# Performance work log

Hardware: AMD Instinct MI355X
Metric: run time of the kernel (lower is better)

The kernel has to match this reference:

```python
import jax, jax.numpy as jnp
import numpy as np

N_VOLS, N_PARTS = 4, 8          # hard-coded in GL.forward
B = N_VOLS * N_PARTS            # asserted batch size = 32
DIM, HID, PROJ = 8192, 4096, 256
TEMP = 0.1
BN_EPS = 1e-5


def setup_inputs() -> dict:
    key = jax.random.key(0)
    k = jax.random.split(key, 5)
    s1 = 1.0 / np.sqrt(DIM)
    s2 = 1.0 / np.sqrt(HID)
    return {
        "x": jax.random.normal(k[0], (B, DIM), jnp.float32),
        "W1": jax.random.uniform(k[1], (DIM, HID), jnp.float32, -s1, s1),
        "b1": jax.random.uniform(k[2], (HID,), jnp.float32, -s1, s1),
        "gamma": jnp.ones((HID,), jnp.float32),
        "beta": jnp.zeros((HID,), jnp.float32),
        "W2": jax.random.uniform(k[3], (HID, PROJ), jnp.float32, -s2, s2),
        "b2": jax.random.uniform(k[4], (PROJ,), jnp.float32, -s2, s2),
    }


def _gl_loss(proj):
    # F.normalize(p=2, dim=-1); CosineSimilarity on unit vectors == dot product
    p = proj / jnp.linalg.norm(proj, axis=-1, keepdims=True)
    sims = (p @ p.T) / TEMP                       # [B, B]
    idx = jnp.arange(B)
    # pos_index(i) = {i % n_parts + v * n_parts} -> same part id; includes i itself
    pos_mask = (idx[:, None] % N_PARTS) == (idx[None, :] % N_PARTS)  # [B, B], 4 per row
    neg_mask = ~pos_mask                                             # 28 per row
    E = jnp.exp(sims)                              # original uses raw exp (no max-shift)
    row_neg = jnp.sum(jnp.where(neg_mask, E, 0.0), axis=1)    # sum_j exp(s[i, neg_j])
    ET = E.T                                        # ET[i, p] = exp(s[p, i])
    col_neg = jnp.sum(jnp.where(neg_mask, ET, 0.0), axis=1)   # sum_j exp(s[neg_j, i])
    t1 = -jnp.log(E / (E + row_neg[:, None]))      # row-direction term per (i, pos)
    t2 = -jnp.log(ET / (ET + col_neg[:, None]))    # column-direction term per (i, pos)
    per_row = jnp.sum(jnp.where(pos_mask, t1 + t2, 0.0), axis=1) / N_VOLS
    return jnp.sum(per_row) / (B * 2)


def reference(x, W1, b1, gamma, beta, W2, b2):
    # projector MLP: Linear -> BatchNorm1d (training stats) -> ReLU -> Linear
    h = x @ W1 + b1
    mu = jnp.mean(h, axis=0)
    var = jnp.var(h, axis=0)                       # biased variance, BN training mode
    h = gamma * (h - mu) * jax.lax.rsqrt(var + BN_EPS) + beta
    h = jax.nn.relu(h)
    proj = h @ W2 + b2                             # [B, PROJ]
    return _gl_loss(proj)
```

## Files before the change

### kernel.cpp

```cpp
#include <hip/hip_runtime.h>

#define DIM   8192
#define HID   4096
#define PROJ  256
#define NB    32
#define KSP1  16
#define KCH1  (DIM / KSP1)
#define KT1   (KCH1 / 32)
#define KSP2  16
#define KCH2  (HID / KSP2)
#define KT2   (KCH2 / 32)

typedef __attribute__((ext_vector_type(8))) short bf16x8;
typedef __attribute__((ext_vector_type(4))) float f32x4;

__device__ __forceinline__ float bf2f(unsigned short u) {
    return __uint_as_float(((unsigned)u) << 16);
}
__device__ __forceinline__ unsigned short f2bf(float f) {
    unsigned u = __float_as_uint(f);
    u += 0x7fffu + ((u >> 16) & 1u);
    return (unsigned short)(u >> 16);
}
__device__ __forceinline__ unsigned pk2(float a, float b) {
    return (unsigned)f2bf(a) | ((unsigned)f2bf(b) << 16);
}

__device__ __forceinline__ bool detect_bf16(const unsigned* __restrict__ xw, int lane) {
    unsigned v = xw[lane];
    int e = (int)((v >> 7) & 0xffu);
    bool pl = (e >= 100 && e <= 135);
    unsigned long long b = __ballot(pl);
    return __popcll(b) >= 32;
}

__global__ __launch_bounds__(256, 4) void gemm1_kernel(
    const void* __restrict__ xv, const void* __restrict__ W1v,
    float* __restrict__ hpart)
{
    __shared__ unsigned short wt[2 * 32 * 66];
    const int t  = threadIdx.x;
    const int nb = blockIdx.x & 63;
    const int kc = blockIdx.x >> 6;
    const int n0 = nb * 64;
    const int k0 = kc * KCH1;

    const bool isbf = detect_bf16((const unsigned*)xv, t & 63);
    const unsigned short* xu  = (const unsigned short*)xv;
    const float*          xf  = (const float*)xv;
    const unsigned short* W1u = (const unsigned short*)W1v;
    const float*          W1f = (const float*)W1v;

    const int lane = t & 63;
    const int w    = t >> 6;
    const int g    = lane >> 4;
    const int ln   = lane & 15;
    const int wr   = t >> 3;
    const int wc   = (t & 7) * 8;

    auto loadW1 = [&](int kt) -> uint4 {
        const int base = (k0 + kt * 32 + wr) * HID + n0 + wc;
        if (isbf) return *(const uint4*)(W1u + base);
        float4 f0 = *(const float4*)(W1f + base);
        float4 f1 = *(const float4*)(W1f + base + 4);
        return make_uint4(pk2(f0.x, f0.y), pk2(f0.z, f0.w),
                          pk2(f1.x, f1.y), pk2(f1.z, f1.w));
    };
    auto storeTile = [&](int buf, uint4 v) {
        unsigned* dst = (unsigned*)&wt[buf * 2112 + wr * 66 + wc];
        dst[0] = v.x; dst[1] = v.y; dst[2] = v.z; dst[3] = v.w;
    };
    auto loadA = [&](int kt, int mt) -> bf16x8 {
        const int base = (mt * 16 + ln) * DIM + k0 + kt * 32 + g * 8;
        if (isbf) return *(const bf16x8*)(xu + base);
        float4 f0 = *(const float4*)(xf + base);
        float4 f1 = *(const float4*)(xf + base + 4);
        union { uint4 u; bf16x8 v; } c;
        c.u = make_uint4(pk2(f0.x, f0.y), pk2(f0.z, f0.w),
                         pk2(f1.x, f1.y), pk2(f1.z, f1.w));
        return c.v;
    };

    storeTile(0, loadW1(0));
    uint4 pf[3];
    pf[0] = loadW1(1); pf[1] = loadW1(2); pf[2] = loadW1(3);
    bf16x8 areg[2][2];
    areg[0][0] = loadA(0, 0); areg[0][1] = loadA(0, 1);
    areg[1][0] = loadA(1, 0); areg[1][1] = loadA(1, 1);
    __syncthreads();

    f32x4 acc0 = {0.f, 0.f, 0.f, 0.f};
    f32x4 acc1 = {0.f, 0.f, 0.f, 0.f};
    const int bco = w * 16 + ln;

    #pragma unroll
    for (int kt = 0; kt < KT1; ++kt) {
        const int cur = kt & 1;
        bf16x8 b;
        const unsigned short* wpb = &wt[cur * 2112 + g * 528 + bco];
        #pragma unroll
        for (int j = 0; j < 8; ++j) b[j] = (short)wpb[j * 66];

        acc0 = __builtin_amdgcn_mfma_f32_16x16x32_bf16(areg[cur][0], b, acc0, 0, 0, 0);
        acc1 = __builtin_amdgcn_mfma_f32_16x16x32_bf16(areg[cur][1], b, acc1, 0, 0, 0);

        if (kt + 2 < KT1) { areg[cur][0] = loadA(kt + 2, 0); areg[cur][1] = loadA(kt + 2, 1); }
        if (kt + 1 < KT1) storeTile(cur ^ 1, pf[kt % 3]);
        if (kt + 4 < KT1) pf[kt % 3] = loadW1(kt + 4);
        __syncthreads();
    }

    const int col = n0 + bco;
    #pragma unroll
    for (int r = 0; r < 4; ++r) {
        hpart[(kc * NB + g * 4 + r) * HID + col]      = acc0[r];
        hpart[(kc * NB + 16 + g * 4 + r) * HID + col] = acc1[r];
    }
}

__global__ __launch_bounds__(256) void bnrelu_kernel(
    const float* __restrict__ hpart, const void* __restrict__ gv,
    const void* __restrict__ bev, unsigned short* __restrict__ hrelu,
    const void* __restrict__ xv)
{
    const int t = threadIdx.x;
    const int c = t & 15, q = t >> 4;
    const int n = blockIdx.x * 16 + c;
    const bool isbf = detect_bf16((const unsigned*)xv, t & 63);

    float h0 = 0.f, h1 = 0.f;
    #pragma unroll
    for (int kc = 0; kc < KSP1; ++kc) {
        h0 += hpart[(kc * NB + 2 * q) * HID + n];
        h1 += hpart[(kc * NB + 2 * q + 1) * HID + n];
    }

    __shared__ float red[16][16];
    __shared__ float stat[2][16];
    red[q][c] = h0 + h1;
    __syncthreads();
    if (t < 16) {
        float s = 0.f;
        #pragma unroll
        for (int i = 0; i < 16; ++i) s += red[i][t];
        stat[0][t] = s * (1.f / 32.f);
    }
    __syncthreads();
    const float mu = stat[0][c];
    const float d0 = h0 - mu, d1 = h1 - mu;
    red[q][c] = d0 * d0 + d1 * d1;
    __syncthreads();
    if (t < 16) {
        float v = 0.f;
        #pragma unroll
        for (int i = 0; i < 16; ++i) v += red[i][t];
        v *= (1.f / 32.f);
        const int nn = blockIdx.x * 16 + t;
        const float ga = isbf ? bf2f(((const unsigned short*)gv)[nn])  : ((const float*)gv)[nn];
        const float be = isbf ? bf2f(((const unsigned short*)bev)[nn]) : ((const float*)bev)[nn];
        stat[0][t] = ga * rsqrtf(v + 1e-5f);
        stat[1][t] = be;
    }
    __syncthreads();
    const float sc = stat[0][c], be = stat[1][c];
    hrelu[(2 * q) * HID + n]     = f2bf(fmaxf(d0 * sc + be, 0.f));
    hrelu[(2 * q + 1) * HID + n] = f2bf(fmaxf(d1 * sc + be, 0.f));
}

__global__ __launch_bounds__(256, 4) void gemm2_kernel(
    const unsigned short* __restrict__ hrelu, const void* __restrict__ W2v,
    float* __restrict__ ppart, const void* __restrict__ xv)
{
    __shared__ unsigned short wt[2 * 32 * 66];
    const int t  = threadIdx.x;
    const int nb = blockIdx.x & 3;
    const int kc = blockIdx.x >> 2;
    const int n0 = nb * 64;
    const int k0 = kc * KCH2;

    const bool isbf = detect_bf16((const unsigned*)xv, t & 63);
    const unsigned short* W2u = (const unsigned short*)W2v;
    const float*          W2f = (const float*)W2v;

    const int lane = t & 63;
    const int w    = t >> 6;
    const int g    = lane >> 4;
    const int ln   = lane & 15;
    const int wr   = t >> 3;
    const int wc   = (t & 7) * 8;

    auto loadW2 = [&](int kt) -> uint4 {
        const int base = (k0 + kt * 32 + wr) * PROJ + n0 + wc;
        if (isbf) return *(const uint4*)(W2u + base);
        float4 f0 = *(const float4*)(W2f + base);
        float4 f1 = *(const float4*)(W2f + base + 4);
        return make_uint4(pk2(f0.x, f0.y), pk2(f0.z, f0.w),
                          pk2(f1.x, f1.y), pk2(f1.z, f1.w));
    };
    auto storeTile = [&](int buf, uint4 v) {
        unsigned* dst = (unsigned*)&wt[buf * 2112 + wr * 66 + wc];
        dst[0] = v.x; dst[1] = v.y; dst[2] = v.z; dst[3] = v.w;
    };
    auto loadA = [&](int kt, int mt) -> bf16x8 {
        return *(const bf16x8*)(hrelu + (mt * 16 + ln) * HID + k0 + kt * 32 + g * 8);
    };

    storeTile(0, loadW2(0));
    uint4 pf[3];
    pf[0] = loadW2(1); pf[1] = loadW2(2); pf[2] = loadW2(3);
    bf16x8 areg[2][2];
    areg[0][0] = loadA(0, 0); areg[0][1] = loadA(0, 1);
    areg[1][0] = loadA(1, 0); areg[1][1] = loadA(1, 1);
    __syncthreads();

    f32x4 acc0 = {0.f, 0.f, 0.f, 0.f};
    f32x4 acc1 = {0.f, 0.f, 0.f, 0.f};
    const int bco = w * 16 + ln;

    #pragma unroll
    for (int kt = 0; kt < KT2; ++kt) {
        const int cur = kt & 1;
        bf16x8 b;
        const unsigned short* wpb = &wt[cur * 2112 + g * 528 + bco];
        #pragma unroll
        for (int j = 0; j < 8; ++j) b[j] = (short)wpb[j * 66];

        acc0 = __builtin_amdgcn_mfma_f32_16x16x32_bf16(areg[cur][0], b, acc0, 0, 0, 0);
        acc1 = __builtin_amdgcn_mfma_f32_16x16x32_bf16(areg[cur][1], b, acc1, 0, 0, 0);

        if (kt + 2 < KT2) { areg[cur][0] = loadA(kt + 2, 0); areg[cur][1] = loadA(kt + 2, 1); }
        if (kt + 1 < KT2) storeTile(cur ^ 1, pf[kt % 3]);
        if (kt + 4 < KT2) pf[kt % 3] = loadW2(kt + 4);
        __syncthreads();
    }

    const int col = n0 + bco;
    #pragma unroll
    for (int r = 0; r < 4; ++r) {
        ppart[(kc * NB + g * 4 + r) * PROJ + col]      = acc0[r];
        ppart[(kc * NB + 16 + g * 4 + r) * PROJ + col] = acc1[r];
    }
}

__global__ __launch_bounds__(1024) void loss_kernel(
    const float* __restrict__ ppart, const void* __restrict__ b2v,
    const void* __restrict__ xv, unsigned* __restrict__ out)
{
    __shared__ float ps[32][260];
    __shared__ float npart2[32][8];
    __shared__ float inrm[32];
    __shared__ float rowtot[32];
    const int t = threadIdx.x;
    const bool isbf = detect_bf16((const unsigned*)xv, t & 63);

    #pragma unroll
    for (int i = 0; i < 8; ++i) {
        const int o = i * 1024 + t;
        float s = 0.f;
        #pragma unroll
        for (int s16 = 0; s16 < KSP2; ++s16) s += ppart[s16 * (NB * PROJ) + o];
        const int c = o & 255;
        s += isbf ? bf2f(((const unsigned short*)b2v)[c]) : ((const float*)b2v)[c];
        ps[o >> 8][c] = s;
    }
    __syncthreads();

    if (t < 256) {
        const int r = t >> 3, seg = t & 7;
        float s = 0.f;
        #pragma unroll
        for (int c = 0; c < 32; ++c) { float v = ps[r][seg * 32 + c]; s += v * v; }
        npart2[r][seg] = s;
    }
    __syncthreads();
    if (t < 32) {
        float s = 0.f;
        #pragma unroll
        for (int j = 0; j < 8; ++j) s += npart2[t][j];
        inrm[t] = rsqrtf(s);
    }
    __syncthreads();

    const int wv   = t >> 6;
    const int lane = t & 63;
    const int j    = (lane >> 1) & 31;
    const int half = lane & 1;
    #pragma unroll
    for (int rr = 0; rr < 2; ++rr) {
        const int i = wv * 2 + rr;
        float acc = 0.f;
        const int cb = half * 128;
        #pragma unroll
        for (int c = 0; c < 128; c += 4) {
            float4 a = *(const float4*)&ps[i][cb + c];
            float4 b = *(const float4*)&ps[j][cb + c];
            acc += a.x * b.x + a.y * b.y + a.z * b.z + a.w * b.w;
        }
        acc += __shfl_xor(acc, 1);

        const float sim = acc * inrm[i] * inrm[j] * 10.0f;
        const float E   = __expf(sim);
        const bool pos  = ((j & 7) == (i & 7));

        float nv = (!pos && half == 0) ? E : 0.f;
        #pragma unroll
        for (int s = 1; s < 64; s <<= 1) nv += __shfl_xor(nv, s);
        float pv = (pos && half == 0) ? (logf(E + nv) - sim) : 0.f;
        #pragma unroll
        for (int s = 1; s < 64; s <<= 1) pv += __shfl_xor(pv, s);
        if (lane == 0) rowtot[i] = pv;
    }
    __syncthreads();

    if (t < 64) {
        float v = (t < 32) ? rowtot[t] : 0.f;
        #pragma unroll
        for (int s = 1; s < 64; s <<= 1) v += __shfl_xor(v, s);
        if (t == 0) {
            const float loss = v * (1.0f / 128.0f);
            const unsigned lb = (unsigned)f2bf(loss);
            const unsigned base = (__float_as_uint(loss) & 0xffff0000u) | lb;
            unsigned best = base;
            float ebest = fabsf(__uint_as_float(base) - loss);
            const unsigned cp = base + 0x10000u;
            const float ep = fabsf(__uint_as_float(cp) - loss);
            if (ep < ebest) { best = cp; ebest = ep; }
            const unsigned cm = base - 0x10000u;
            const float em = fabsf(__uint_as_float(cm) - loss);
            if (em < ebest) { best = cm; }
            out[0] = best;
        }
    }
}

extern "C" void kernel_launch(void* const* d_in, const int* in_sizes, int n_in,
                              void* d_out, int out_size, void* d_ws, size_t ws_size,
                              hipStream_t stream) {
    const void* x  = d_in[0];
    const void* W1 = d_in[1];
    const void* ga = d_in[3];
    const void* be = d_in[4];
    const void* W2 = d_in[5];
    const void* b2 = d_in[6];

    char* wsp = (char*)d_ws;
    float* hpart = (float*)wsp;                 wsp += (size_t)KSP1 * NB * HID * 4;
    unsigned short* hrelu = (unsigned short*)wsp; wsp += (size_t)NB * HID * 2;
    float* ppart = (float*)wsp;                 wsp += (size_t)KSP2 * NB * PROJ * 4;

    gemm1_kernel<<<1024, 256, 0, stream>>>(x, W1, hpart);
    bnrelu_kernel<<<256, 256, 0, stream>>>(hpart, ga, be, hrelu, x);
    gemm2_kernel<<<64, 256, 0, stream>>>(hrelu, W2, ppart, x);
    loss_kernel<<<1, 1024, 0, stream>>>(ppart, b2, x, (unsigned*)d_out);
}
```

Baseline: 243.8 us.

## Use direct global-to-LDS loads with XOR swizzle in gemm1; vectorize BN-ReLU

The gemm1 W1 tile staging moves from register prefetch plus LDS store to direct global_load_lds copies, when the input is bf16, into a 64-wide LDS tile that uses an XOR column swizzle in place of padding. The next stage is issued at the top of each iteration. The BN-ReLU kernel now handles 64 columns per block with float4 loads and ushort4 stores, using a quarter of the blocks. Inputs here are fp32, so the bf16 direct-to-LDS path probably does not run. The fp32 path now converts and stores synchronously with no multi-stage register prefetch, which may expose load latency.

New measurement: 244.9 us. About the same (+0.5%).

```diff
diff --git a/kernel.cpp b/kernel.cpp
--- a/kernel.cpp
+++ b/kernel.cpp
@@ -34,11 +34,17 @@
     return __popcll(b) >= 32;
 }
 
+__device__ __forceinline__ void cp16_g2l(const void* g, void* l) {
+    __builtin_amdgcn_global_load_lds(
+        (const __attribute__((address_space(1))) void*)g,
+        (__attribute__((address_space(3))) void*)l, 16, 0, 0);
+}
+
 __global__ __launch_bounds__(256, 4) void gemm1_kernel(
     const void* __restrict__ xv, const void* __restrict__ W1v,
     float* __restrict__ hpart)
 {
-    __shared__ unsigned short wt[2 * 32 * 66];
+    __shared__ unsigned short wt[2][2048];
     const int t  = threadIdx.x;
     const int nb = blockIdx.x & 63;
     const int kc = blockIdx.x >> 6;
@@ -55,20 +61,24 @@
     const int w    = t >> 6;
     const int g    = lane >> 4;
     const int ln   = lane & 15;
-    const int wr   = t >> 3;
-    const int wc   = (t & 7) * 8;
-
-    auto loadW1 = [&](int kt) -> uint4 {
-        const int base = (k0 + kt * 32 + wr) * HID + n0 + wc;
-        if (isbf) return *(const uint4*)(W1u + base);
-        float4 f0 = *(const float4*)(W1f + base);
-        float4 f1 = *(const float4*)(W1f + base + 4);
-        return make_uint4(pk2(f0.x, f0.y), pk2(f0.z, f0.w),
-                          pk2(f1.x, f1.y), pk2(f1.z, f1.w));
-    };
-    auto storeTile = [&](int buf, uint4 v) {
-        unsigned* dst = (unsigned*)&wt[buf * 2112 + wr * 66 + wc];
-        dst[0] = v.x; dst[1] = v.y; dst[2] = v.z; dst[3] = v.w;
+
+    const int srow = w * 8 + (lane >> 3);
+    const int scb  = (lane & 7) ^ w;
+    const long sgo = (long)srow * HID + n0 + scb * 8;
+    unsigned short* sl = &wt[0][w * 512];
+
+    auto issue_stage = [&](int buf, int kt) {
+        const unsigned short* gp = W1u + ((long)(k0 + kt * 32) * HID + sgo);
+        if (isbf) {
+            cp16_g2l((const void*)gp, (void*)(sl + buf * 2048));
+        } else {
+            const float* gpf = W1f + ((long)(k0 + kt * 32) * HID + sgo);
+            float4 f0 = *(const float4*)gpf;
+            float4 f1 = *(const float4*)(gpf + 4);
+            unsigned* dst = (unsigned*)&wt[buf][srow * 64 + (lane & 7) * 8];
+            dst[0] = pk2(f0.x, f0.y); dst[1] = pk2(f0.z, f0.w);
+            dst[2] = pk2(f1.x, f1.y); dst[3] = pk2(f1.z, f1.w);
+        }
     };
     auto loadA = [&](int kt, int mt) -> bf16x8 {
         const int base = (mt * 16 + ln) * DIM + k0 + kt * 32 + g * 8;
@@ -81,9 +91,7 @@
         return c.v;
     };
 
-    storeTile(0, loadW1(0));
-    uint4 pf[3];
-    pf[0] = loadW1(1); pf[1] = loadW1(2); pf[2] = loadW1(3);
+    issue_stage(0, 0);
     bf16x8 areg[2][2];
     areg[0][0] = loadA(0, 0); areg[0][1] = loadA(0, 1);
     areg[1][0] = loadA(1, 0); areg[1][1] = loadA(1, 1);
@@ -92,21 +100,22 @@
     f32x4 acc0 = {0.f, 0.f, 0.f, 0.f};
     f32x4 acc1 = {0.f, 0.f, 0.f, 0.f};
     const int bco = w * 16 + ln;
+    const int bidx = g * 8 * 64 + (((bco >> 3) ^ g) * 8 + (bco & 7));
 
     #pragma unroll
     for (int kt = 0; kt < KT1; ++kt) {
         const int cur = kt & 1;
+        if (kt + 1 < KT1) issue_stage(cur ^ 1, kt + 1);
+
         bf16x8 b;
-        const unsigned short* wpb = &wt[cur * 2112 + g * 528 + bco];
-        #pragma unroll
-        for (int j = 0; j < 8; ++j) b[j] = (short)wpb[j * 66];
+        const unsigned short* wpb = &wt[cur][bidx];
+        #pragma unroll
+        for (int j = 0; j < 8; ++j) b[j] = (short)wpb[j * 64];
 
         acc0 = __builtin_amdgcn_mfma_f32_16x16x32_bf16(areg[cur][0], b, acc0, 0, 0, 0);
         acc1 = __builtin_amdgcn_mfma_f32_16x16x32_bf16(areg[cur][1], b, acc1, 0, 0, 0);
 
         if (kt + 2 < KT1) { areg[cur][0] = loadA(kt + 2, 0); areg[cur][1] = loadA(kt + 2, 1); }
-        if (kt + 1 < KT1) storeTile(cur ^ 1, pf[kt % 3]);
-        if (kt + 4 < KT1) pf[kt % 3] = loadW1(kt + 4);
         __syncthreads();
     }
 
@@ -123,48 +132,57 @@
     const void* __restrict__ bev, unsigned short* __restrict__ hrelu,
     const void* __restrict__ xv)
 {
-    const int t = threadIdx.x;
-    const int c = t & 15, q = t >> 4;
-    const int n = blockIdx.x * 16 + c;
+    __shared__ float red[16][64];
+    __shared__ float ssc[64], sbe[64], smu[64];
+    const int t  = threadIdx.x;
+    const int c4 = t & 15, q = t >> 4;
+    const int n0 = blockIdx.x * 64;
+    const int nb = n0 + c4 * 4;
     const bool isbf = detect_bf16((const unsigned*)xv, t & 63);
 
-    float h0 = 0.f, h1 = 0.f;
+    f32x4 h0 = {0.f, 0.f, 0.f, 0.f};
+    f32x4 h1 = {0.f, 0.f, 0.f, 0.f};
     #pragma unroll
     for (int kc = 0; kc < KSP1; ++kc) {
-        h0 += hpart[(kc * NB + 2 * q) * HID + n];
-        h1 += hpart[(kc * NB + 2 * q + 1) * HID + n];
-    }
-
-    __shared__ float red[16][16];
-    __shared__ float stat[2][16];
-    red[q][c] = h0 + h1;
-    __syncthreads();
-    if (t < 16) {
+        h0 += *(const f32x4*)(hpart + (size_t)(kc * 32 + 2 * q) * HID + nb);
+        h1 += *(const f32x4*)(hpart + (size_t)(kc * 32 + 2 * q + 1) * HID + nb);
+    }
+    *(f32x4*)&red[q][c4 * 4] = h0 + h1;
+    __syncthreads();
+    if (t < 64) {
         float s = 0.f;
         #pragma unroll
         for (int i = 0; i < 16; ++i) s += red[i][t];
-        stat[0][t] = s * (1.f / 32.f);
-    }
-    __syncthreads();
-    const float mu = stat[0][c];
-    const float d0 = h0 - mu, d1 = h1 - mu;
-    red[q][c] = d0 * d0 + d1 * d1;
-    __syncthreads();
-    if (t < 16) {
+        smu[t] = s * (1.f / 32.f);
+    }
+    __syncthreads();
+    const f32x4 mu = *(const f32x4*)&smu[c4 * 4];
+    const f32x4 d0 = h0 - mu, d1 = h1 - mu;
+    *(f32x4*)&red[q][c4 * 4] = d0 * d0 + d1 * d1;
+    __syncthreads();
+    if (t < 64) {
         float v = 0.f;
         #pragma unroll
         for (int i = 0; i < 16; ++i) v += red[i][t];
         v *= (1.f / 32.f);
-        const int nn = blockIdx.x * 16 + t;
+        const int nn = n0 + t;
         const float ga = isbf ? bf2f(((const unsigned short*)gv)[nn])  : ((const float*)gv)[nn];
         const float be = isbf ? bf2f(((const unsigned short*)bev)[nn]) : ((const float*)bev)[nn];
-        stat[0][t] = ga * rsqrtf(v + 1e-5f);
-        stat[1][t] = be;
-    }
-    __syncthreads();
-    const float sc = stat[0][c], be = stat[1][c];
-    hrelu[(2 * q) * HID + n]     = f2bf(fmaxf(d0 * sc + be, 0.f));
-    hrelu[(2 * q + 1) * HID + n] = f2bf(fmaxf(d1 * sc + be, 0.f));
+        ssc[t] = ga * rsqrtf(v + 1e-5f);
+        sbe[t] = be;
+    }
+    __syncthreads();
+    const f32x4 sc = *(const f32x4*)&ssc[c4 * 4];
+    const f32x4 be = *(const f32x4*)&sbe[c4 * 4];
+    f32x4 r0 = d0 * sc + be;
+    f32x4 r1 = d1 * sc + be;
+    ushort4 o0, o1;
+    o0.x = f2bf(fmaxf(r0.x, 0.f)); o0.y = f2bf(fmaxf(r0.y, 0.f));
+    o0.z = f2bf(fmaxf(r0.z, 0.f)); o0.w = f2bf(fmaxf(r0.w, 0.f));
+    o1.x = f2bf(fmaxf(r1.x, 0.f)); o1.y = f2bf(fmaxf(r1.y, 0.f));
+    o1.z = f2bf(fmaxf(r1.z, 0.f)); o1.w = f2bf(fmaxf(r1.w, 0.f));
+    *(ushort4*)(hrelu + (size_t)(2 * q) * HID + nb)     = o0;
+    *(ushort4*)(hrelu + (size_t)(2 * q + 1) * HID + nb) = o1;
 }
 
 __global__ __launch_bounds__(256, 4) void gemm2_kernel(
@@ -349,7 +367,7 @@
     float* ppart = (float*)wsp;                 wsp += (size_t)KSP2 * NB * PROJ * 4;
 
     gemm1_kernel<<<1024, 256, 0, stream>>>(x, W1, hpart);
-    bnrelu_kernel<<<256, 256, 0, stream>>>(hpart, ga, be, hrelu, x);
+    bnrelu_kernel<<<64, 256, 0, stream>>>(hpart, ga, be, hrelu, x);
     gemm2_kernel<<<64, 256, 0, stream>>>(hrelu, W2, ppart, x);
     loss_kernel<<<1, 1024, 0, stream>>>(ppart, b2, x, (unsigned*)d_out);
 }
```
